# Kernel tuning notes

Hardware: AMD Instinct MI355X
Metric: run time of the kernel (lower is better)

The kernel has to match this reference:

```python
import jax, jax.numpy as jnp
import numpy as np

B, T, D = 16, 4096, 768          # batch, tokens, hidden
N_BOX = 1024                      # total boxes across batch
MAX_BBOX = 128                    # cfg.MODEL.MAX_BBOX_NUM
DIM_DETR = 256                    # DETR feature dim (features[:,1:])


def _lin(k, din, dout):
    kw, kb = jax.random.split(k)
    s = 1.0 / np.sqrt(din)
    W = jax.random.uniform(kw, (dout, din), minval=-s, maxval=s, dtype=jnp.float32)
    b = jax.random.uniform(kb, (dout,), minval=-s, maxval=s, dtype=jnp.float32)
    return W, b


def setup_inputs() -> dict:
    key = jax.random.key(0)
    ks = jax.random.split(key, 10)
    inputs = jax.random.normal(ks[0], (B, T, D), dtype=jnp.float32)
    img = jnp.sort(jax.random.randint(ks[1], (N_BOX,), 0, B))
    rest = jax.random.randint(ks[2], (N_BOX, 4), 0, 224)
    bboxes = jnp.concatenate([img[:, None], rest], axis=1).astype(jnp.int32)
    features = jax.random.normal(ks[3], (N_BOX, 1 + DIM_DETR), dtype=jnp.float32)
    t1w, t1b = _lin(ks[4], D, D)      # transform layer 1
    t2w, t2b = _lin(ks[5], D, D)      # transform layer 2
    d1w, d1b = _lin(ks[6], D, D)      # deep_trans layer 1
    d2w, d2b = _lin(ks[7], D, D)      # deep_trans layer 2
    k8a, k8b = jax.random.split(ks[8])
    m1w, m1b = _lin(k8a, DIM_DETR, D) # mlp layer 1 (256->768)
    m2w, m2b = _lin(k8b, D, D)        # mlp layer 2
    pw, pb = _lin(ks[9], 2 * D, D)    # projection (1536->768)
    return dict(inputs=inputs, bboxes=bboxes, features=features,
                t1w=t1w, t1b=t1b, t2w=t2w, t2b=t2b,
                d1w=d1w, d1b=d1b, d2w=d2w, d2b=d2b,
                m1w=m1w, m1b=m1b, m2w=m2w, m2b=m2b,
                pw=pw, pb=pb)


def reference(inputs, bboxes, features, t1w, t1b, t2w, t2b,
              d1w, d1b, d2w, d2b, m1w, m1b, m2w, m2b, pw, pb):
    x = inputs.mean(axis=1)                                    # [B, D]
    ret_x = jax.nn.relu(x @ d1w.T + d1b) @ d2w.T + d2b         # deep_trans
    xt = jax.nn.relu(x @ t1w.T + t1b) @ t2w.T + t2b            # transform
    img = bboxes[:, 0]                                          # [N] image idx per box
    x_boxes = xt[img]                                           # broadcast image feat to its boxes
    fm = jax.nn.relu(features[:, 1:] @ m1w.T + m1b) @ m2w.T + m2b  # DETR mlp
    h = jnp.concatenate([x_boxes, fm], axis=1) @ pw.T + pb      # [N, D]
    # ragged pad: scatter each box into slot (img, rank-within-image)
    counts = jax.ops.segment_sum(jnp.ones((N_BOX,), jnp.int32), img, num_segments=B)
    offsets = jnp.cumsum(counts) - counts                       # exclusive cumsum (boxes sorted by img)
    pos = jnp.arange(N_BOX) - offsets[img]
    vis_output = jnp.zeros((B, MAX_BBOX, D), h.dtype).at[img, pos].set(h)
    att_mask = (jnp.arange(MAX_BBOX)[None, :] < counts[:, None]).astype(jnp.float32)
    return vis_output, att_mask, ret_x
```

## Files before the change

### kernel.cpp

```cpp
#include <hip/hip_runtime.h>

#define B_ 16
#define T_ 4096
#define D_ 768
#define NBOX 1024
#define MAXBB 128
#define DDETR 256

typedef unsigned short u16;
typedef short bf16x8 __attribute__((ext_vector_type(8)));
typedef float f32x4 __attribute__((ext_vector_type(4)));

__device__ __forceinline__ void split_bf(float f, u16& h, u16& l) {
    unsigned u = __builtin_bit_cast(unsigned, f);
    unsigned r = u + 0x7fffu + ((u >> 16) & 1u);
    u16 hb = (u16)(r >> 16);
    float hf = __builtin_bit_cast(float, (unsigned)hb << 16);
    float lf = f - hf;
    unsigned ul = __builtin_bit_cast(unsigned, lf);
    unsigned rl = ul + 0x7fffu + ((ul >> 16) & 1u);
    h = hb; l = (u16)(rl >> 16);
}

__global__ __launch_bounds__(192) void k_mean_partial(const float4* __restrict__ in4,
                                                      float4* __restrict__ part4) {
    int blk = blockIdx.x;
    int b = blk >> 6, c = blk & 63;
    int t = threadIdx.x;
    const float4* base = in4 + (size_t)b * (T_ * D_ / 4) + (size_t)c * (64 * D_ / 4);
    float4 s = {0.f, 0.f, 0.f, 0.f};
    #pragma unroll 4
    for (int r = 0; r < 64; ++r) {
        float4 v = base[(size_t)r * 192 + t];
        s.x += v.x; s.y += v.y; s.z += v.z; s.w += v.w;
    }
    part4[(size_t)blk * 192 + t] = s;
}

__global__ __launch_bounds__(96) void k_mean_final_pack(const float* __restrict__ part,
                                                        u16* __restrict__ xph, u16* __restrict__ xpl) {
    int b = blockIdx.x;
    int kc = threadIdx.x;
    f32x4 s0 = {0,0,0,0}, s1 = {0,0,0,0};
    for (int c = 0; c < 64; ++c) {
        const float* p = part + ((size_t)(b * 64 + c)) * D_ + kc * 8;
        s0 += *(const f32x4*)p;
        s1 += *(const f32x4*)(p + 4);
    }
    const float inv = 1.0f / T_;
    bf16x8 hv, lv;
    #pragma unroll
    for (int j = 0; j < 4; ++j) {
        u16 h, l;
        split_bf(s0[j] * inv, h, l); hv[j] = (short)h; lv[j] = (short)l;
        split_bf(s1[j] * inv, h, l); hv[4 + j] = (short)h; lv[4 + j] = (short)l;
    }
    size_t off = ((size_t)kc * 16 + b) * 8;
    *(bf16x8*)(xph + off) = hv;
    *(bf16x8*)(xpl + off) = lv;
}

struct WDesc { const float* src; u16* hi; u16* lo; int N; int K; };
struct WPack7 { WDesc d[7]; };

__global__ __launch_bounds__(256) void k_pack_w(WPack7 ws) {
    WDesc d = ws.d[blockIdx.y];
    int idx = blockIdx.x * 256 + threadIdx.x;
    int Kc = d.K >> 3;
    int total = d.N * Kc;
    if (idx >= total) return;
    int n = idx / Kc, kc = idx - n * Kc;
    const float* s = d.src + (size_t)n * d.K + kc * 8;
    f32x4 v0 = *(const f32x4*)s, v1 = *(const f32x4*)(s + 4);
    bf16x8 hv, lv;
    #pragma unroll
    for (int j = 0; j < 4; ++j) {
        u16 h, l;
        split_bf(v0[j], h, l); hv[j] = (short)h; lv[j] = (short)l;
        split_bf(v1[j], h, l); hv[4 + j] = (short)h; lv[4 + j] = (short)l;
    }
    size_t off = ((size_t)(n >> 4) * Kc + kc) * 128 + (n & 15) * 8;
    *(bf16x8*)(d.hi + off) = hv;
    *(bf16x8*)(d.lo + off) = lv;
}

__global__ __launch_bounds__(256) void k_pack_feat(const float* __restrict__ feat,
                                                   u16* __restrict__ fh, u16* __restrict__ fl) {
    int idx = blockIdx.x * 256 + threadIdx.x;
    if (idx >= NBOX * 32) return;
    int i = idx >> 5, kc = idx & 31;
    const float* s = feat + (size_t)i * 257 + 1 + kc * 8;
    bf16x8 hv, lv;
    #pragma unroll
    for (int j = 0; j < 8; ++j) {
        u16 h, l;
        split_bf(s[j], h, l); hv[j] = (short)h; lv[j] = (short)l;
    }
    size_t off = ((size_t)(i >> 4) * 32 + kc) * 128 + (i & 15) * 8;
    *(bf16x8*)(fh + off) = hv;
    *(bf16x8*)(fl + off) = lv;
}

__global__ __launch_bounds__(256) void k_mfma(const u16* __restrict__ Ahi, const u16* __restrict__ Alo,
                                              const u16* __restrict__ Whi, const u16* __restrict__ Wlo,
                                              float* __restrict__ P, int Kc, int kcLen, int nks) {
    int z = blockIdx.z;
    int term = z / nks, ks = z - term * nks;
    const u16* A = (term == 2) ? Alo : Ahi;
    const u16* W = (term == 1) ? Wlo : Whi;
    int lane = threadIdx.x & 63, w = threadIdx.x >> 6;
    int wm = w >> 1, wn = w & 1;
    int mt0 = blockIdx.y * 8 + wm * 4;
    int nt0 = blockIdx.x * 8 + wn * 4;
    int kc0 = ks * kcLen;
    int nk = kcLen >> 2;

    const u16* Ap = A + ((size_t)mt0 * Kc + kc0) * 128 + lane * 8;
    const u16* Wp = W + ((size_t)nt0 * Kc + kc0) * 128 + lane * 8;
    size_t astr = (size_t)Kc * 128;

    bf16x8 a[4], b[4];
    #pragma unroll
    for (int i = 0; i < 4; ++i) {
        a[i] = *(const bf16x8*)(Ap + i * astr);
        b[i] = *(const bf16x8*)(Wp + i * astr);
    }
    f32x4 acc[16];
    #pragma unroll
    for (int i = 0; i < 16; ++i) acc[i] = (f32x4){0.f, 0.f, 0.f, 0.f};

    for (int k = 0; k < nk; ++k) {
        bf16x8 an[4], bn[4];
        if (k + 1 < nk) {
            #pragma unroll
            for (int i = 0; i < 4; ++i) {
                an[i] = *(const bf16x8*)(Ap + i * astr + (size_t)(k + 1) * 512);
                bn[i] = *(const bf16x8*)(Wp + i * astr + (size_t)(k + 1) * 512);
            }
        }
        #pragma unroll
        for (int i = 0; i < 4; ++i)
            #pragma unroll
            for (int j = 0; j < 4; ++j)
                acc[i * 4 + j] = __builtin_amdgcn_mfma_f32_16x16x32_bf16(a[i], b[j], acc[i * 4 + j], 0, 0, 0);
        #pragma unroll
        for (int i = 0; i < 4; ++i) { a[i] = an[i]; b[i] = bn[i]; }
    }

    float* Pz = P + (size_t)z * (1024 * 768);
    int rb = (lane >> 4) * 4, cb = lane & 15;
    #pragma unroll
    for (int i = 0; i < 4; ++i)
        #pragma unroll
        for (int j = 0; j < 4; ++j) {
            int row = (mt0 + i) * 16 + rb;
            int col = (nt0 + j) * 16 + cb;
            float* p = Pz + (size_t)row * 768 + col;
            f32x4 v = acc[i * 4 + j];
            #pragma unroll
            for (int r = 0; r < 4; ++r) p[(size_t)r * 768] = v[r];
        }
}

template<int RELU>
__global__ __launch_bounds__(256) void k_epi_pack(const float* __restrict__ P, int NS,
                                                  const float* __restrict__ bias,
                                                  u16* __restrict__ dhi, u16* __restrict__ dlo,
                                                  int KcDst, int kcOff) {
    int idx = blockIdx.x * 256 + threadIdx.x;
    int m = idx / 96, kc = idx - m * 96;
    const float* p0 = P + (size_t)m * 768 + kc * 8;
    f32x4 s0 = *(const f32x4*)p0, s1 = *(const f32x4*)(p0 + 4);
    for (int z = 1; z < NS; ++z) {
        const float* p = p0 + (size_t)z * (1024 * 768);
        s0 += *(const f32x4*)p; s1 += *(const f32x4*)(p + 4);
    }
    s0 += *(const f32x4*)(bias + kc * 8);
    s1 += *(const f32x4*)(bias + kc * 8 + 4);
    bf16x8 hv, lv;
    #pragma unroll
    for (int j = 0; j < 4; ++j) {
        float v0 = RELU ? fmaxf(s0[j], 0.f) : s0[j];
        float v1 = RELU ? fmaxf(s1[j], 0.f) : s1[j];
        u16 h, l;
        split_bf(v0, h, l); hv[j] = (short)h; lv[j] = (short)l;
        split_bf(v1, h, l); hv[4 + j] = (short)h; lv[4 + j] = (short)l;
    }
    size_t off = ((size_t)(m >> 4) * KcDst + kcOff + kc) * 128 + (m & 15) * 8;
    *(bf16x8*)(dhi + off) = hv;
    *(bf16x8*)(dlo + off) = lv;
}

__global__ __launch_bounds__(256) void k_epi_f32(const float* __restrict__ P, int NS,
                                                 const float* __restrict__ bias,
                                                 float* __restrict__ C) {
    int idx = blockIdx.x * 256 + threadIdx.x;
    int m = idx / 192, c4 = idx - m * 192;
    size_t off = (size_t)m * 768 + c4 * 4;
    f32x4 s = *(const f32x4*)(P + off);
    for (int z = 1; z < NS; ++z) s += *(const f32x4*)(P + (size_t)z * (1024 * 768) + off);
    s += *(const f32x4*)(bias + c4 * 4);
    *(f32x4*)(C + off) = s;
}

__global__ __launch_bounds__(256) void k_small(const u16* __restrict__ A0h, const u16* __restrict__ A0l,
                                               const u16* __restrict__ A1h, const u16* __restrict__ A1l,
                                               const u16* __restrict__ W0h, const u16* __restrict__ W0l,
                                               const u16* __restrict__ W1h, const u16* __restrict__ W1l,
                                               float* __restrict__ Ps) {
    int z = blockIdx.y;
    int term = z >> 2, ks = z & 3;
    int lane = threadIdx.x & 63, w = threadIdx.x >> 6;
    int nt0 = blockIdx.x * 16 + w * 4;
    int path = nt0 >= 48;
    int ntp = nt0 - path * 48;
    const u16* Ah = path ? A1h : A0h;
    const u16* Al = path ? A1l : A0l;
    const u16* Wh = path ? W1h : W0h;
    const u16* Wl = path ? W1l : W0l;
    const u16* A = (term == 2) ? Al : Ah;
    const u16* W = (term == 1) ? Wl : Wh;
    int kc0 = ks * 24;

    const u16* Ap = A + (size_t)kc0 * 128 + lane * 8;
    const u16* Wp = W + ((size_t)ntp * 96 + kc0) * 128 + lane * 8;

    f32x4 acc[4];
    #pragma unroll
    for (int i = 0; i < 4; ++i) acc[i] = (f32x4){0.f, 0.f, 0.f, 0.f};

    #pragma unroll
    for (int k = 0; k < 6; ++k) {
        bf16x8 a = *(const bf16x8*)(Ap + (size_t)k * 512);
        bf16x8 b[4];
        #pragma unroll
        for (int j = 0; j < 4; ++j)
            b[j] = *(const bf16x8*)(Wp + (size_t)j * 96 * 128 + (size_t)k * 512);
        #pragma unroll
        for (int j = 0; j < 4; ++j)
            acc[j] = __builtin_amdgcn_mfma_f32_16x16x32_bf16(a, b[j], acc[j], 0, 0, 0);
    }

    float* Pz = Ps + (size_t)z * (16 * 1536);
    int rb = (lane >> 4) * 4, cb = lane & 15;
    #pragma unroll
    for (int j = 0; j < 4; ++j) {
        int col = (nt0 + j) * 16 + cb;
        float* p = Pz + (size_t)rb * 1536 + col;
        f32x4 v = acc[j];
        #pragma unroll
        for (int r = 0; r < 4; ++r) p[(size_t)r * 1536] = v[r];
    }
}

__global__ __launch_bounds__(256) void k_sepi1(const float* __restrict__ Ps,
                                               const float* __restrict__ d1b, const float* __restrict__ t1b,
                                               u16* __restrict__ xh, u16* __restrict__ xl) {
    int idx = blockIdx.x * 256 + threadIdx.x;
    int r = idx / 192, cc = idx - r * 192;
    size_t base = (size_t)r * 1536 + cc * 8;
    f32x4 s0 = {0,0,0,0}, s1 = {0,0,0,0};
    for (int z = 0; z < 12; ++z) {
        const float* p = Ps + (size_t)z * (16 * 1536) + base;
        s0 += *(const f32x4*)p; s1 += *(const f32x4*)(p + 4);
    }
    int path = cc >= 96;
    int ccp = cc - path * 96;
    const float* bias = (path ? t1b : d1b) + ccp * 8;
    s0 += *(const f32x4*)bias;
    s1 += *(const f32x4*)(bias + 4);
    bf16x8 hv, lv;
    #pragma unroll
    for (int j = 0; j < 4; ++j) {
        u16 h, l;
        split_bf(fmaxf(s0[j], 0.f), h, l); hv[j] = (short)h; lv[j] = (short)l;
        split_bf(fmaxf(s1[j], 0.f), h, l); hv[4 + j] = (short)h; lv[4 + j] = (short)l;
    }
    size_t off = (size_t)path * 12288 + (size_t)ccp * 128 + r * 8;
    *(bf16x8*)(xh + off) = hv;
    *(bf16x8*)(xl + off) = lv;
}

__global__ __launch_bounds__(256) void k_sepi2(const float* __restrict__ Ps,
                                               const float* __restrict__ d2b, const float* __restrict__ t2b,
                                               float* __restrict__ retx,
                                               u16* __restrict__ xth, u16* __restrict__ xtl) {
    int idx = blockIdx.x * 256 + threadIdx.x;
    int r = idx / 192, cc = idx - r * 192;
    size_t base = (size_t)r * 1536 + cc * 8;
    f32x4 s0 = {0,0,0,0}, s1 = {0,0,0,0};
    for (int z = 0; z < 12; ++z) {
        const float* p = Ps + (size_t)z * (16 * 1536) + base;
        s0 += *(const f32x4*)p; s1 += *(const f32x4*)(p + 4);
    }
    int path = cc >= 96;
    int ccp = cc - path * 96;
    const float* bias = (path ? t2b : d2b) + ccp * 8;
    s0 += *(const f32x4*)bias;
    s1 += *(const f32x4*)(bias + 4);
    if (!path) {
        float* o = retx + (size_t)r * 768 + ccp * 8;
        *(f32x4*)o = s0;
        *(f32x4*)(o + 4) = s1;
    } else {
        bf16x8 hv, lv;
        #pragma unroll
        for (int j = 0; j < 4; ++j) {
            u16 h, l;
            split_bf(s0[j], h, l); hv[j] = (short)h; lv[j] = (short)l;
            split_bf(s1[j], h, l); hv[4 + j] = (short)h; lv[4 + j] = (short)l;
        }
        size_t off = (size_t)ccp * 128 + r * 8;
        *(bf16x8*)(xth + off) = hv;
        *(bf16x8*)(xtl + off) = lv;
    }
}

__global__ __launch_bounds__(256) void k_gather_pack(const u16* __restrict__ xth, const u16* __restrict__ xtl,
                                                     const int* __restrict__ bboxes,
                                                     u16* __restrict__ hxh, u16* __restrict__ hxl) {
    int idx = blockIdx.x * 256 + threadIdx.x;
    int i = idx / 96, kc = idx - i * 96;
    int img = bboxes[i * 5];
    size_t soff = ((size_t)kc * 16 + img) * 8;
    size_t doff = ((size_t)(i >> 4) * 192 + kc) * 128 + (i & 15) * 8;
    *(bf16x8*)(hxh + doff) = *(const bf16x8*)(xth + soff);
    *(bf16x8*)(hxl + doff) = *(const bf16x8*)(xtl + soff);
}

__global__ __launch_bounds__(256) void k_meta(const int* __restrict__ bboxes,
                                              int* __restrict__ cnt_g, int* __restrict__ off_g,
                                              float* __restrict__ att) {
    __shared__ int cnt[B_];
    __shared__ int off[B_];
    int tid = threadIdx.x;
    if (tid < B_) cnt[tid] = 0;
    __syncthreads();
    for (int i = tid; i < NBOX; i += 256) atomicAdd(&cnt[bboxes[i * 5]], 1);
    __syncthreads();
    if (tid == 0) {
        int acc = 0;
        for (int b = 0; b < B_; ++b) { off[b] = acc; acc += cnt[b]; }
    }
    __syncthreads();
    if (tid < B_) { cnt_g[tid] = cnt[tid]; off_g[tid] = off[tid]; }
    for (int j = tid; j < B_ * MAXBB; j += 256) {
        int b = j >> 7, p = j & 127;
        att[j] = (p < cnt[b]) ? 1.0f : 0.0f;
    }
}

__global__ __launch_bounds__(256) void k_vis(const float* __restrict__ h,
                                             const int* __restrict__ cnt,
                                             const int* __restrict__ off,
                                             float* __restrict__ vis) {
    int idx = blockIdx.x * 256 + threadIdx.x;
    int slot = idx / 192, d = idx - slot * 192;
    int b = slot >> 7, p = slot & 127;
    float4 v = {0.f, 0.f, 0.f, 0.f};
    if (p < cnt[b]) v = *(const float4*)&h[(size_t)(off[b] + p) * D_ + d * 4];
    *(float4*)&vis[(size_t)slot * D_ + d * 4] = v;
}

extern "C" void kernel_launch(void* const* d_in, const int* in_sizes, int n_in,
                              void* d_out, int out_size, void* d_ws, size_t ws_size,
                              hipStream_t stream) {
    const float* inputs   = (const float*)d_in[0];
    const int*   bboxes   = (const int*)d_in[1];
    const float* features = (const float*)d_in[2];
    const float* t1w = (const float*)d_in[3];
    const float* t1b = (const float*)d_in[4];
    const float* t2w = (const float*)d_in[5];
    const float* t2b = (const float*)d_in[6];
    const float* d1w = (const float*)d_in[7];
    const float* d1b = (const float*)d_in[8];
    const float* d2w = (const float*)d_in[9];
    const float* d2b = (const float*)d_in[10];
    const float* m1w = (const float*)d_in[11];
    const float* m1b = (const float*)d_in[12];
    const float* m2w = (const float*)d_in[13];
    const float* m2b = (const float*)d_in[14];
    const float* pw  = (const float*)d_in[15];
    const float* pb  = (const float*)d_in[16];

    float* out  = (float*)d_out;
    float* vis  = out;
    float* att  = out + 1572864;
    float* retx = out + 1574912;

    float* wsf  = (float*)d_ws;
    float* part = wsf;
    float* P    = wsf + 786432;
    float* Ps   = P + 12 * 786432;
    float* h    = Ps + 294912;
    int*   cnt  = (int*)(h + 786432);
    int*   off  = cnt + 16;
    u16*   sb   = (u16*)(off + 48);

    u16* t1wh = sb;              u16* t1wl = t1wh + 589824;
    u16* t2wh = t1wl + 589824;   u16* t2wl = t2wh + 589824;
    u16* d1wh = t2wl + 589824;   u16* d1wl = d1wh + 589824;
    u16* d2wh = d1wl + 589824;   u16* d2wl = d2wh + 589824;
    u16* m1wh = d2wl + 589824;   u16* m1wl = m1wh + 196608;
    u16* m2wh = m1wl + 196608;   u16* m2wl = m2wh + 589824;
    u16* pwh  = m2wl + 589824;   u16* pwl  = pwh + 1179648;
    u16* feah = pwl + 1179648;   u16* feal = feah + 262144;
    u16* fm1h = feal + 262144;   u16* fm1l = fm1h + 786432;
    u16* hxh  = fm1l + 786432;   u16* hxl  = hxh + 1572864;
    u16* xph  = hxl + 1572864;   u16* xpl  = xph + 12288;
    u16* xch  = xpl + 12288;     u16* xcl  = xch + 24576;
    u16* xth  = xcl + 24576;     u16* xtl  = xth + 12288;

    k_meta<<<1, 256, 0, stream>>>(bboxes, cnt, off, att);

    k_mean_partial<<<B_ * 64, 192, 0, stream>>>((const float4*)inputs, (float4*)part);
    k_mean_final_pack<<<16, 96, 0, stream>>>(part, xph, xpl);

    WPack7 wp;
    wp.d[0] = {t1w, t1wh, t1wl, 768, 768};
    wp.d[1] = {t2w, t2wh, t2wl, 768, 768};
    wp.d[2] = {d1w, d1wh, d1wl, 768, 768};
    wp.d[3] = {d2w, d2wh, d2wl, 768, 768};
    wp.d[4] = {m1w, m1wh, m1wl, 768, 256};
    wp.d[5] = {m2w, m2wh, m2wl, 768, 768};
    wp.d[6] = {pw,  pwh,  pwl,  768, 1536};
    k_pack_w<<<dim3(576, 7), 256, 0, stream>>>(wp);
    k_pack_feat<<<128, 256, 0, stream>>>(features, feah, feal);

    k_small<<<dim3(6, 12), 256, 0, stream>>>(xph, xpl, xph, xpl,
                                             d1wh, d1wl, t1wh, t1wl, Ps);
    k_sepi1<<<12, 256, 0, stream>>>(Ps, d1b, t1b, xch, xcl);
    k_small<<<dim3(6, 12), 256, 0, stream>>>(xch, xcl, xch + 12288, xcl + 12288,
                                             d2wh, d2wl, t2wh, t2wl, Ps);
    k_sepi2<<<12, 256, 0, stream>>>(Ps, d2b, t2b, retx, xth, xtl);

    k_gather_pack<<<384, 256, 0, stream>>>(xth, xtl, bboxes, hxh, hxl);

    k_mfma<<<dim3(6, 8, 6), 256, 0, stream>>>(feah, feal, m1wh, m1wl, P, 32, 16, 2);
    k_epi_pack<1><<<384, 256, 0, stream>>>(P, 6, m1b, fm1h, fm1l, 96, 0);

    k_mfma<<<dim3(6, 8, 12), 256, 0, stream>>>(fm1h, fm1l, m2wh, m2wl, P, 96, 24, 4);
    k_epi_pack<0><<<384, 256, 0, stream>>>(P, 12, m2b, hxh, hxl, 192, 96);

    k_mfma<<<dim3(6, 8, 12), 256, 0, stream>>>(hxh, hxl, pwh, pwl, P, 192, 48, 4);
    k_epi_f32<<<768, 256, 0, stream>>>(P, 12, pb, h);

    k_vis<<<1536, 256, 0, stream>>>(h, cnt, off, vis);
}
```

Before: 426.1 us.

## Fuse packing kernels, gather xt inside projection GEMM, scatter directly into vis

Result: faster. 408.8 us (-4.1%).

```diff
diff --git a/kernel.cpp b/kernel.cpp
--- a/kernel.cpp
+++ b/kernel.cpp
@@ -37,77 +37,74 @@
     part4[(size_t)blk * 192 + t] = s;
 }
 
-__global__ __launch_bounds__(96) void k_mean_final_pack(const float* __restrict__ part,
-                                                        u16* __restrict__ xph, u16* __restrict__ xpl) {
-    int b = blockIdx.x;
-    int kc = threadIdx.x;
-    f32x4 s0 = {0,0,0,0}, s1 = {0,0,0,0};
-    for (int c = 0; c < 64; ++c) {
-        const float* p = part + ((size_t)(b * 64 + c)) * D_ + kc * 8;
-        s0 += *(const f32x4*)p;
-        s1 += *(const f32x4*)(p + 4);
-    }
-    const float inv = 1.0f / T_;
-    bf16x8 hv, lv;
-    #pragma unroll
-    for (int j = 0; j < 4; ++j) {
-        u16 h, l;
-        split_bf(s0[j] * inv, h, l); hv[j] = (short)h; lv[j] = (short)l;
-        split_bf(s1[j] * inv, h, l); hv[4 + j] = (short)h; lv[4 + j] = (short)l;
-    }
-    size_t off = ((size_t)kc * 16 + b) * 8;
-    *(bf16x8*)(xph + off) = hv;
-    *(bf16x8*)(xpl + off) = lv;
-}
-
-struct WDesc { const float* src; u16* hi; u16* lo; int N; int K; };
-struct WPack7 { WDesc d[7]; };
-
-__global__ __launch_bounds__(256) void k_pack_w(WPack7 ws) {
+struct WDesc { const float* src; u16* hi; u16* lo; int N; int K; int stride; int vec; };
+struct WPack8 { WDesc d[8]; };
+
+__global__ __launch_bounds__(256) void k_pack_all(WPack8 ws, const float* __restrict__ part,
+                                                  u16* __restrict__ xph, u16* __restrict__ xpl) {
+    __shared__ float xm[768];
+    if (blockIdx.y == 8) {
+        if (blockIdx.x >= 16) return;
+        int b = blockIdx.x;
+        int t = threadIdx.x;
+        if (t < 192) {
+            f32x4 s = {0.f, 0.f, 0.f, 0.f};
+            #pragma unroll 4
+            for (int c = 0; c < 64; ++c)
+                s += *(const f32x4*)(part + ((size_t)(b * 64 + c)) * 768 + t * 4);
+            s *= (1.0f / T_);
+            *(f32x4*)(xm + t * 4) = s;
+        }
+        __syncthreads();
+        if (t < 96) {
+            const float* p = xm + t * 8;
+            bf16x8 hv, lv;
+            #pragma unroll
+            for (int j = 0; j < 8; ++j) {
+                u16 h, l;
+                split_bf(p[j], h, l); hv[j] = (short)h; lv[j] = (short)l;
+            }
+            size_t off = ((size_t)t * 16 + b) * 8;
+            *(bf16x8*)(xph + off) = hv;
+            *(bf16x8*)(xpl + off) = lv;
+        }
+        return;
+    }
     WDesc d = ws.d[blockIdx.y];
     int idx = blockIdx.x * 256 + threadIdx.x;
     int Kc = d.K >> 3;
     int total = d.N * Kc;
     if (idx >= total) return;
     int n = idx / Kc, kc = idx - n * Kc;
-    const float* s = d.src + (size_t)n * d.K + kc * 8;
-    f32x4 v0 = *(const f32x4*)s, v1 = *(const f32x4*)(s + 4);
+    const float* s = d.src + (size_t)n * d.stride + kc * 8;
+    float v[8];
+    if (d.vec) {
+        f32x4 v0 = *(const f32x4*)s, v1 = *(const f32x4*)(s + 4);
+        #pragma unroll
+        for (int j = 0; j < 4; ++j) { v[j] = v0[j]; v[4 + j] = v1[j]; }
+    } else {
+        #pragma unroll
+        for (int j = 0; j < 8; ++j) v[j] = s[j];
+    }
     bf16x8 hv, lv;
     #pragma unroll
-    for (int j = 0; j < 4; ++j) {
+    for (int j = 0; j < 8; ++j) {
         u16 h, l;
-        split_bf(v0[j], h, l); hv[j] = (short)h; lv[j] = (short)l;
-        split_bf(v1[j], h, l); hv[4 + j] = (short)h; lv[4 + j] = (short)l;
+        split_bf(v[j], h, l); hv[j] = (short)h; lv[j] = (short)l;
     }
     size_t off = ((size_t)(n >> 4) * Kc + kc) * 128 + (n & 15) * 8;
     *(bf16x8*)(d.hi + off) = hv;
     *(bf16x8*)(d.lo + off) = lv;
 }
 
-__global__ __launch_bounds__(256) void k_pack_feat(const float* __restrict__ feat,
-                                                   u16* __restrict__ fh, u16* __restrict__ fl) {
-    int idx = blockIdx.x * 256 + threadIdx.x;
-    if (idx >= NBOX * 32) return;
-    int i = idx >> 5, kc = idx & 31;
-    const float* s = feat + (size_t)i * 257 + 1 + kc * 8;
-    bf16x8 hv, lv;
-    #pragma unroll
-    for (int j = 0; j < 8; ++j) {
-        u16 h, l;
-        split_bf(s[j], h, l); hv[j] = (short)h; lv[j] = (short)l;
-    }
-    size_t off = ((size_t)(i >> 4) * 32 + kc) * 128 + (i & 15) * 8;
-    *(bf16x8*)(fh + off) = hv;
-    *(bf16x8*)(fl + off) = lv;
-}
-
+template<int GATHER>
 __global__ __launch_bounds__(256) void k_mfma(const u16* __restrict__ Ahi, const u16* __restrict__ Alo,
                                               const u16* __restrict__ Whi, const u16* __restrict__ Wlo,
+                                              const u16* __restrict__ Xth, const u16* __restrict__ Xtl,
+                                              const int* __restrict__ bbx,
                                               float* __restrict__ P, int Kc, int kcLen, int nks) {
     int z = blockIdx.z;
     int term = z / nks, ks = z - term * nks;
-    const u16* A = (term == 2) ? Alo : Ahi;
-    const u16* W = (term == 1) ? Wlo : Whi;
     int lane = threadIdx.x & 63, w = threadIdx.x >> 6;
     int wm = w >> 1, wn = w & 1;
     int mt0 = blockIdx.y * 8 + wm * 4;
@@ -115,15 +112,33 @@
     int kc0 = ks * kcLen;
     int nk = kcLen >> 2;
 
-    const u16* Ap = A + ((size_t)mt0 * Kc + kc0) * 128 + lane * 8;
+    const u16* W = (term == 1) ? Wlo : Whi;
     const u16* Wp = W + ((size_t)nt0 * Kc + kc0) * 128 + lane * 8;
-    size_t astr = (size_t)Kc * 128;
+    size_t wstr = (size_t)Kc * 128;
+
+    const u16* Abase;
+    size_t aofs[4];
+    if (GATHER && ks == 0) {
+        Abase = (term == 2) ? Xtl : Xth;
+        #pragma unroll
+        for (int i = 0; i < 4; ++i) {
+            int row = (mt0 + i) * 16 + (lane & 15);
+            aofs[i] = (size_t)(lane >> 4) * 128 + (size_t)bbx[row * 5] * 8;
+        }
+    } else {
+        int AKc = GATHER ? 96 : Kc;
+        int kc0a = GATHER ? 0 : kc0;
+        Abase = (term == 2) ? Alo : Ahi;
+        #pragma unroll
+        for (int i = 0; i < 4; ++i)
+            aofs[i] = ((size_t)(mt0 + i) * AKc + kc0a) * 128 + lane * 8;
+    }
 
     bf16x8 a[4], b[4];
     #pragma unroll
     for (int i = 0; i < 4; ++i) {
-        a[i] = *(const bf16x8*)(Ap + i * astr);
-        b[i] = *(const bf16x8*)(Wp + i * astr);
+        a[i] = *(const bf16x8*)(Abase + aofs[i]);
+        b[i] = *(const bf16x8*)(Wp + i * wstr);
     }
     f32x4 acc[16];
     #pragma unroll
@@ -134,8 +149,8 @@
         if (k + 1 < nk) {
             #pragma unroll
             for (int i = 0; i < 4; ++i) {
-                an[i] = *(const bf16x8*)(Ap + i * astr + (size_t)(k + 1) * 512);
-                bn[i] = *(const bf16x8*)(Wp + i * astr + (size_t)(k + 1) * 512);
+                an[i] = *(const bf16x8*)(Abase + aofs[i] + (size_t)(k + 1) * 512);
+                bn[i] = *(const bf16x8*)(Wp + i * wstr + (size_t)(k + 1) * 512);
             }
         }
         #pragma unroll
@@ -191,16 +206,21 @@
     *(bf16x8*)(dlo + off) = lv;
 }
 
-__global__ __launch_bounds__(256) void k_epi_f32(const float* __restrict__ P, int NS,
+__global__ __launch_bounds__(256) void k_epi_vis(const float* __restrict__ P, int NS,
                                                  const float* __restrict__ bias,
-                                                 float* __restrict__ C) {
+                                                 float* __restrict__ vis,
+                                                 const int* __restrict__ bbx,
+                                                 const int* __restrict__ off) {
     int idx = blockIdx.x * 256 + threadIdx.x;
     int m = idx / 192, c4 = idx - m * 192;
-    size_t off = (size_t)m * 768 + c4 * 4;
-    f32x4 s = *(const f32x4*)(P + off);
-    for (int z = 1; z < NS; ++z) s += *(const f32x4*)(P + (size_t)z * (1024 * 768) + off);
+    size_t o = (size_t)m * 768 + c4 * 4;
+    f32x4 s = *(const f32x4*)(P + o);
+    for (int z = 1; z < NS; ++z) s += *(const f32x4*)(P + (size_t)z * (1024 * 768) + o);
     s += *(const f32x4*)(bias + c4 * 4);
-    *(f32x4*)(C + off) = s;
+    int b = bbx[m * 5];
+    int pp = m - off[b];
+    if (pp < MAXBB)
+        *(f32x4*)&vis[((size_t)(b * MAXBB + pp)) * 768 + c4 * 4] = s;
 }
 
 __global__ __launch_bounds__(256) void k_small(const u16* __restrict__ A0h, const u16* __restrict__ A0l,
@@ -316,21 +336,14 @@
     }
 }
 
-__global__ __launch_bounds__(256) void k_gather_pack(const u16* __restrict__ xth, const u16* __restrict__ xtl,
-                                                     const int* __restrict__ bboxes,
-                                                     u16* __restrict__ hxh, u16* __restrict__ hxl) {
-    int idx = blockIdx.x * 256 + threadIdx.x;
-    int i = idx / 96, kc = idx - i * 96;
-    int img = bboxes[i * 5];
-    size_t soff = ((size_t)kc * 16 + img) * 8;
-    size_t doff = ((size_t)(i >> 4) * 192 + kc) * 128 + (i & 15) * 8;
-    *(bf16x8*)(hxh + doff) = *(const bf16x8*)(xth + soff);
-    *(bf16x8*)(hxl + doff) = *(const bf16x8*)(xtl + soff);
-}
-
-__global__ __launch_bounds__(256) void k_meta(const int* __restrict__ bboxes,
-                                              int* __restrict__ cnt_g, int* __restrict__ off_g,
-                                              float* __restrict__ att) {
+__global__ __launch_bounds__(256) void k_meta_vz(const int* __restrict__ bboxes,
+                                                 int* __restrict__ cnt_g, int* __restrict__ off_g,
+                                                 float* __restrict__ att, f32x4* __restrict__ vis4) {
+    if (blockIdx.x > 0) {
+        int idx = (blockIdx.x - 1) * 256 + threadIdx.x;
+        vis4[idx] = (f32x4){0.f, 0.f, 0.f, 0.f};
+        return;
+    }
     __shared__ int cnt[B_];
     __shared__ int off[B_];
     int tid = threadIdx.x;
@@ -348,18 +361,6 @@
         int b = j >> 7, p = j & 127;
         att[j] = (p < cnt[b]) ? 1.0f : 0.0f;
     }
-}
-
-__global__ __launch_bounds__(256) void k_vis(const float* __restrict__ h,
-                                             const int* __restrict__ cnt,
-                                             const int* __restrict__ off,
-                                             float* __restrict__ vis) {
-    int idx = blockIdx.x * 256 + threadIdx.x;
-    int slot = idx / 192, d = idx - slot * 192;
-    int b = slot >> 7, p = slot & 127;
-    float4 v = {0.f, 0.f, 0.f, 0.f};
-    if (p < cnt[b]) v = *(const float4*)&h[(size_t)(off[b] + p) * D_ + d * 4];
-    *(float4*)&vis[(size_t)slot * D_ + d * 4] = v;
 }
 
 extern "C" void kernel_launch(void* const* d_in, const int* in_sizes, int n_in,
@@ -391,9 +392,8 @@
     float* wsf  = (float*)d_ws;
     float* part = wsf;
     float* P    = wsf + 786432;
-    float* Ps   = P + 12 * 786432;
-    float* h    = Ps + 294912;
-    int*   cnt  = (int*)(h + 786432);
+    float* Ps   = P + 6 * 786432;
+    int*   cnt  = (int*)(Ps + 294912);
     int*   off  = cnt + 16;
     u16*   sb   = (u16*)(off + 48);
 
@@ -406,26 +406,25 @@
     u16* pwh  = m2wl + 589824;   u16* pwl  = pwh + 1179648;
     u16* feah = pwl + 1179648;   u16* feal = feah + 262144;
     u16* fm1h = feal + 262144;   u16* fm1l = fm1h + 786432;
-    u16* hxh  = fm1l + 786432;   u16* hxl  = hxh + 1572864;
-    u16* xph  = hxl + 1572864;   u16* xpl  = xph + 12288;
+    u16* fmh  = fm1l + 786432;   u16* fml  = fmh + 786432;
+    u16* xph  = fml + 786432;    u16* xpl  = xph + 12288;
     u16* xch  = xpl + 12288;     u16* xcl  = xch + 24576;
     u16* xth  = xcl + 24576;     u16* xtl  = xth + 12288;
 
-    k_meta<<<1, 256, 0, stream>>>(bboxes, cnt, off, att);
+    k_meta_vz<<<1537, 256, 0, stream>>>(bboxes, cnt, off, att, (f32x4*)vis);
 
     k_mean_partial<<<B_ * 64, 192, 0, stream>>>((const float4*)inputs, (float4*)part);
-    k_mean_final_pack<<<16, 96, 0, stream>>>(part, xph, xpl);
-
-    WPack7 wp;
-    wp.d[0] = {t1w, t1wh, t1wl, 768, 768};
-    wp.d[1] = {t2w, t2wh, t2wl, 768, 768};
-    wp.d[2] = {d1w, d1wh, d1wl, 768, 768};
-    wp.d[3] = {d2w, d2wh, d2wl, 768, 768};
-    wp.d[4] = {m1w, m1wh, m1wl, 768, 256};
-    wp.d[5] = {m2w, m2wh, m2wl, 768, 768};
-    wp.d[6] = {pw,  pwh,  pwl,  768, 1536};
-    k_pack_w<<<dim3(576, 7), 256, 0, stream>>>(wp);
-    k_pack_feat<<<128, 256, 0, stream>>>(features, feah, feal);
+
+    WPack8 wp;
+    wp.d[0] = {t1w, t1wh, t1wl, 768, 768, 768, 1};
+    wp.d[1] = {t2w, t2wh, t2wl, 768, 768, 768, 1};
+    wp.d[2] = {d1w, d1wh, d1wl, 768, 768, 768, 1};
+    wp.d[3] = {d2w, d2wh, d2wl, 768, 768, 768, 1};
+    wp.d[4] = {m1w, m1wh, m1wl, 768, 256, 256, 1};
+    wp.d[5] = {m2w, m2wh, m2wl, 768, 768, 768, 1};
+    wp.d[6] = {pw,  pwh,  pwl,  768, 1536, 1536, 1};
+    wp.d[7] = {features + 1, feah, feal, 1024, 256, 257, 0};
+    k_pack_all<<<dim3(576, 9), 256, 0, stream>>>(wp, part, xph, xpl);
 
     k_small<<<dim3(6, 12), 256, 0, stream>>>(xph, xpl, xph, xpl,
                                              d1wh, d1wl, t1wh, t1wl, Ps);
@@ -434,16 +433,15 @@
                                              d2wh, d2wl, t2wh, t2wl, Ps);
     k_sepi2<<<12, 256, 0, stream>>>(Ps, d2b, t2b, retx, xth, xtl);
 
-    k_gather_pack<<<384, 256, 0, stream>>>(xth, xtl, bboxes, hxh, hxl);
-
-    k_mfma<<<dim3(6, 8, 6), 256, 0, stream>>>(feah, feal, m1wh, m1wl, P, 32, 16, 2);
-    k_epi_pack<1><<<384, 256, 0, stream>>>(P, 6, m1b, fm1h, fm1l, 96, 0);
-
-    k_mfma<<<dim3(6, 8, 12), 256, 0, stream>>>(fm1h, fm1l, m2wh, m2wl, P, 96, 24, 4);
-    k_epi_pack<0><<<384, 256, 0, stream>>>(P, 12, m2b, hxh, hxl, 192, 96);
-
-    k_mfma<<<dim3(6, 8, 12), 256, 0, stream>>>(hxh, hxl, pwh, pwl, P, 192, 48, 4);
-    k_epi_f32<<<768, 256, 0, stream>>>(P, 12, pb, h);
-
-    k_vis<<<1536, 256, 0, stream>>>(h, cnt, off, vis);
-}
+    k_mfma<0><<<dim3(6, 8, 3), 256, 0, stream>>>(feah, feal, m1wh, m1wl,
+                                                 nullptr, nullptr, nullptr, P, 32, 32, 1);
+    k_epi_pack<1><<<384, 256, 0, stream>>>(P, 3, m1b, fm1h, fm1l, 96, 0);
+
+    k_mfma<0><<<dim3(6, 8, 6), 256, 0, stream>>>(fm1h, fm1l, m2wh, m2wl,
+                                                 nullptr, nullptr, nullptr, P, 96, 48, 2);
+    k_epi_pack<0><<<384, 256, 0, stream>>>(P, 6, m2b, fmh, fml, 96, 0);
+
+    k_mfma<1><<<dim3(6, 8, 6), 256, 0, stream>>>(fmh, fml, pwh, pwl,
+                                                 xth, xtl, bboxes, P, 192, 96, 2);
+    k_epi_vis<<<768, 256, 0, stream>>>(P, 6, pb, vis, bboxes, off);
+}
```
